# Performance work log

Hardware: AMD Instinct MI355X
Metric: run time of the kernel (lower is better)

## Reference

```python
import jax, jax.numpy as jnp
import numpy as np
import math

EMBED_DIM = 512
NUM_HEADS = 8
HEAD_DIM = EMBED_DIM // NUM_HEADS


def setup_inputs() -> dict:
    key = jax.random.key(0)
    ks = jax.random.split(key, 11)
    s = 1.0 / math.sqrt(EMBED_DIM)
    x = jax.random.normal(ks[0], (8, EMBED_DIM, 32, 32), dtype=jnp.float32)
    Wq = jax.random.uniform(ks[1], (EMBED_DIM, EMBED_DIM), jnp.float32, -s, s)
    bq = jax.random.uniform(ks[2], (EMBED_DIM,), jnp.float32, -s, s)
    Wk = jax.random.uniform(ks[3], (EMBED_DIM, EMBED_DIM), jnp.float32, -s, s)
    bk = jax.random.uniform(ks[4], (EMBED_DIM,), jnp.float32, -s, s)
    Wv = jax.random.uniform(ks[5], (EMBED_DIM, EMBED_DIM), jnp.float32, -s, s)
    bv = jax.random.uniform(ks[6], (EMBED_DIM,), jnp.float32, -s, s)
    Wo = jax.random.uniform(ks[7], (EMBED_DIM, EMBED_DIM), jnp.float32, -s, s)
    bo = jax.random.uniform(ks[8], (EMBED_DIM,), jnp.float32, -s, s)
    gamma = jnp.ones((EMBED_DIM,), jnp.float32)
    beta = jnp.zeros((EMBED_DIM,), jnp.float32)
    return {"x": x, "Wq": Wq, "bq": bq, "Wk": Wk, "bk": bk, "Wv": Wv,
            "bv": bv, "Wo": Wo, "bo": bo, "gamma": gamma, "beta": beta}


def layer_norm(x, gamma, beta, eps=1e-5):
    mu = jnp.mean(x, axis=-1, keepdims=True)
    var = jnp.mean(jnp.square(x - mu), axis=-1, keepdims=True)
    return (x - mu) * jax.lax.rsqrt(var + eps) * gamma + beta


def reference(x, Wq, bq, Wk, bk, Wv, bv, Wo, bo, gamma, beta):
    B, C, H, W = x.shape
    S = H * W
    # [B, S, C]
    x_flat = x.reshape(B, C, S).transpose(0, 2, 1)
    residual = x_flat
    xn = layer_norm(x_flat, gamma, beta)
    # torch Linear: y = x @ W^T + b
    q = (xn @ Wq.T + bq).reshape(B, S, NUM_HEADS, HEAD_DIM)
    k = (xn @ Wk.T + bk).reshape(B, S, NUM_HEADS, HEAD_DIM)
    v = (xn @ Wv.T + bv).reshape(B, S, NUM_HEADS, HEAD_DIM)
    scale = 1.0 / math.sqrt(HEAD_DIM)
    scores = jnp.einsum('bqhd,bkhd->bhqk', q, k) * scale
    attn = jax.nn.softmax(scores, axis=-1)  # dropout is identity in eval
    out = jnp.einsum('bhqk,bkhd->bqhd', attn, v).reshape(B, S, C)
    out = out @ Wo.T + bo + residual
    return out.transpose(0, 2, 1).reshape(B, C, H, W)
```

## Files before the change

kernel.cpp:

```cpp
#include <hip/hip_runtime.h>
#include <hip/hip_bf16.h>

typedef __bf16 bf16_t;
typedef __bf16 bf16x8 __attribute__((ext_vector_type(8)));
typedef float floatx4 __attribute__((ext_vector_type(4)));

#define EMBED 512
#define S_LEN 1024
#define NH 8
#define HD 64
#define LDK 1056
#define LDV 1088

#define MFMA16(a, b, c) __builtin_amdgcn_mfma_f32_16x16x32_bf16(a, b, c, 0, 0, 0)

static __device__ __forceinline__ bf16_t f2bf(float f) {
    unsigned int x = __builtin_bit_cast(unsigned int, f);
    unsigned int lsb = (x >> 16) & 1u;
    x += 0x7fffu + lsb;
    unsigned short u = (unsigned short)(x >> 16);
    return __builtin_bit_cast(bf16_t, u);
}
static __device__ __forceinline__ float bf2f(bf16_t v) {
    unsigned short u = __builtin_bit_cast(unsigned short, v);
    unsigned int x = ((unsigned int)u) << 16;
    return __builtin_bit_cast(float, x);
}
static __device__ __forceinline__ unsigned int pack2(float lo, float hi) {
    return (__builtin_bit_cast(unsigned int, lo) >> 16) |
           (__builtin_bit_cast(unsigned int, hi) & 0xFFFF0000u);
}
static __device__ __forceinline__ unsigned int pack2r(float lo, float hi) {
    unsigned short a = __builtin_bit_cast(unsigned short, f2bf(lo));
    unsigned short b = __builtin_bit_cast(unsigned short, f2bf(hi));
    return (unsigned int)a | ((unsigned int)b << 16);
}

__global__ __launch_bounds__(256) void cvt4_kernel(const float* __restrict__ s0,
                                                   const float* __restrict__ s1,
                                                   const float* __restrict__ s2,
                                                   const float* __restrict__ s3,
                                                   bf16_t* __restrict__ d0,
                                                   bf16_t* __restrict__ d1,
                                                   bf16_t* __restrict__ d2,
                                                   bf16_t* __restrict__ d3) {
    const float* s; bf16_t* d;
    switch (blockIdx.y) {
        case 0:  s = s0; d = d0; break;
        case 1:  s = s1; d = d1; break;
        case 2:  s = s2; d = d2; break;
        default: s = s3; d = d3; break;
    }
    int i = (blockIdx.x * 256 + threadIdx.x) * 8;
#pragma unroll
    for (int j = 0; j < 8; ++j) d[i + j] = f2bf(s[i + j]);
}

__global__ __launch_bounds__(256) void ln_fused_kernel(const float* __restrict__ x,
                                                       const float* __restrict__ gamma,
                                                       const float* __restrict__ beta,
                                                       bf16_t* __restrict__ xn) {
    __shared__ float T[32][521];
    __shared__ float Pm[32][33], Pq[32][33];
    __shared__ float Mu[32], Rs[32];
    int bid = blockIdx.x;
    int b = bid >> 5, s0 = (bid & 31) * 32;
    int t = threadIdx.x;
    int lc = t >> 3;
    int si = (t & 7) * 4;
    const float* xp = x + ((size_t)b * EMBED + lc) * S_LEN + s0 + si;
    float sm[4] = {}, sq[4] = {};
#pragma unroll
    for (int p = 0; p < 16; ++p) {
        int c = lc + p * 32;
        float4 v = *(const float4*)(xp + (size_t)p * 32 * S_LEN);
        int cs = c ^ ((c >> 3) & 0x38);
        T[si + 0][cs] = v.x; T[si + 1][cs] = v.y;
        T[si + 2][cs] = v.z; T[si + 3][cs] = v.w;
        sm[0] += v.x; sq[0] += v.x * v.x;
        sm[1] += v.y; sq[1] += v.y * v.y;
        sm[2] += v.z; sq[2] += v.z * v.z;
        sm[3] += v.w; sq[3] += v.w * v.w;
    }
#pragma unroll
    for (int k = 0; k < 4; ++k) { Pm[si + k][lc] = sm[k]; Pq[si + k][lc] = sq[k]; }
    __syncthreads();
    if (t < 32) {
        float m = 0.f, q = 0.f;
#pragma unroll
        for (int j = 0; j < 32; ++j) { m += Pm[t][j]; q += Pq[t][j]; }
        float mu = m * (1.0f / EMBED);
        float var = q * (1.0f / EMBED) - mu * mu;
        Mu[t] = mu; Rs[t] = rsqrtf(var + 1e-5f);
    }
    __syncthreads();
    int cidx = t & 31;
    int rw = t >> 5;
#pragma unroll
    for (int rg = 0; rg < 4; ++rg) {
        int srl = rg * 8 + rw;
        float mu = Mu[srl], rs = Rs[srl];
        int cb = cidx * 16;
        bf16_t* dst = xn + ((size_t)b * S_LEN + s0 + srl) * EMBED + cb;
#pragma unroll
        for (int h = 0; h < 2; ++h) {
            int c0h = cb + h * 8;
            float4 g0 = *(const float4*)(gamma + c0h);
            float4 g1 = *(const float4*)(gamma + c0h + 4);
            float4 be0 = *(const float4*)(beta + c0h);
            float4 be1 = *(const float4*)(beta + c0h + 4);
            float gv[8] = {g0.x, g0.y, g0.z, g0.w, g1.x, g1.y, g1.z, g1.w};
            float bv[8] = {be0.x, be0.y, be0.z, be0.w, be1.x, be1.y, be1.z, be1.w};
            bf16x8 o;
#pragma unroll
            for (int j = 0; j < 8; ++j) {
                int c = c0h + j;
                int cs = c ^ ((c >> 3) & 0x38);
                o[j] = f2bf((T[srl][cs] - mu) * rs * gv[j] + bv[j]);
            }
            *(bf16x8*)(dst + h * 8) = o;
        }
    }
}

__global__ __launch_bounds__(256) void gemm_kernel(const bf16_t* __restrict__ X,
                                                   const bf16_t* __restrict__ W,
                                                   const float* __restrict__ b0,
                                                   const float* __restrict__ b1,
                                                   const float* __restrict__ b2,
                                                   bf16_t* __restrict__ Y,
                                                   bf16_t* __restrict__ vtb) {
    __shared__ __align__(16) bf16_t Wl[2][128 * 72];
    int t = threadIdx.x;
    int col0 = blockIdx.y * 128, row0 = blockIdx.x * 128;
    int scol = t >> 1, sseg = (t & 1) * 32;
    const bf16_t* wsrc = W + (size_t)(col0 + scol) * EMBED + sseg;
    {
        bf16x8 r0 = *(const bf16x8*)(wsrc);
        bf16x8 r1 = *(const bf16x8*)(wsrc + 8);
        bf16x8 r2 = *(const bf16x8*)(wsrc + 16);
        bf16x8 r3 = *(const bf16x8*)(wsrc + 24);
        bf16_t* d = &Wl[0][scol * 72 + sseg];
        *(bf16x8*)d = r0;        *(bf16x8*)(d + 8) = r1;
        *(bf16x8*)(d + 16) = r2; *(bf16x8*)(d + 24) = r3;
    }
    int lane = t & 63, w = t >> 6, g = lane >> 4, n16 = lane & 15;
    int rw0 = row0 + w * 32;
    const bf16_t* xr0 = X + (size_t)(rw0 + n16) * EMBED + g * 8;
    const bf16_t* xr1 = xr0 + (size_t)16 * EMBED;
    bf16x8 a00 = *(const bf16x8*)(xr0);
    bf16x8 a01 = *(const bf16x8*)(xr0 + 32);
    bf16x8 a10 = *(const bf16x8*)(xr1);
    bf16x8 a11 = *(const bf16x8*)(xr1 + 32);
    __syncthreads();
    floatx4 acc[2][8] = {};
#pragma unroll
    for (int kc = 0; kc < 8; ++kc) {
        bf16x8 p0, p1, p2, p3, na00, na01, na10, na11;
        if (kc < 7) {
            int ko = (kc + 1) * 64;
            p0 = *(const bf16x8*)(wsrc + ko);
            p1 = *(const bf16x8*)(wsrc + ko + 8);
            p2 = *(const bf16x8*)(wsrc + ko + 16);
            p3 = *(const bf16x8*)(wsrc + ko + 24);
            na00 = *(const bf16x8*)(xr0 + ko);
            na01 = *(const bf16x8*)(xr0 + ko + 32);
            na10 = *(const bf16x8*)(xr1 + ko);
            na11 = *(const bf16x8*)(xr1 + ko + 32);
        }
        const bf16_t* wl = &Wl[kc & 1][0];
#pragma unroll
        for (int kk = 0; kk < 2; ++kk) {
            bf16x8 s0 = (kk == 0) ? a00 : a01;
            bf16x8 s1 = (kk == 0) ? a10 : a11;
#pragma unroll
            for (int nt = 0; nt < 8; ++nt) {
                bf16x8 bfr = *(const bf16x8*)(&wl[(nt * 16 + n16) * 72 + kk * 32 + g * 8]);
                acc[0][nt] = MFMA16(s0, bfr, acc[0][nt]);
                acc[1][nt] = MFMA16(s1, bfr, acc[1][nt]);
            }
        }
        if (kc < 7) {
            bf16_t* d = &Wl[(kc + 1) & 1][scol * 72 + sseg];
            *(bf16x8*)d = p0;        *(bf16x8*)(d + 8) = p1;
            *(bf16x8*)(d + 16) = p2; *(bf16x8*)(d + 24) = p3;
            a00 = na00; a01 = na01; a10 = na10; a11 = na11;
        }
        __syncthreads();
    }
    if (col0 < 1024) {
        const float* bp = (col0 < 512) ? b0 : b1;
#pragma unroll
        for (int ar = 0; ar < 2; ++ar)
#pragma unroll
            for (int nt = 0; nt < 8; ++nt) {
                int col = col0 + nt * 16 + n16;
                float bv = bp[col & 511];
#pragma unroll
                for (int r = 0; r < 4; ++r) {
                    int row = rw0 + ar * 16 + g * 4 + r;
                    Y[(size_t)row * LDK + col] = f2bf(acc[ar][nt][r] + bv);
                }
            }
    } else {
        bf16_t* Tl = &Wl[0][0];
#pragma unroll
        for (int ar = 0; ar < 2; ++ar)
#pragma unroll
            for (int nt = 0; nt < 8; ++nt) {
                int chl = nt * 16 + n16;
                float bv = b2[(col0 & 511) + chl];
                uint2 pr;
                pr.x = pack2r(acc[ar][nt][0] + bv, acc[ar][nt][1] + bv);
                pr.y = pack2r(acc[ar][nt][2] + bv, acc[ar][nt][3] + bv);
                *(uint2*)(&Tl[chl * 136 + w * 32 + ar * 16 + g * 4]) = pr;
            }
        __syncthreads();
        int ch = t >> 1, seg = (t & 1) * 64;
        int bb = row0 >> 10, s0 = row0 & 1023;
        bf16_t* dst = vtb + ((size_t)(bb * EMBED + (col0 - 1024) + ch)) * LDV + s0 + seg;
        const bf16_t* srcl = &Tl[ch * 136 + seg];
#pragma unroll
        for (int i = 0; i < 8; ++i)
            *(bf16x8*)(dst + i * 8) = *(const bf16x8*)(srcl + i * 8);
    }
}

__global__ __launch_bounds__(256) void wsgemm_out_kernel(const bf16_t* __restrict__ Wb,
                                                         const bf16_t* __restrict__ act,
                                                         const float* __restrict__ bias,
                                                         const float* __restrict__ xres,
                                                         float* __restrict__ out) {
    __shared__ __align__(16) bf16_t Al[2][64 * 72];
    int b = blockIdx.z, n0 = blockIdx.x * 64, m0 = blockIdx.y * 128;
    int t = threadIdx.x;
    int srow = t >> 2, sseg = (t & 3) * 16;
    const bf16_t* asrc = act + ((size_t)b * S_LEN + n0 + srow) * EMBED + sseg;
    {
        bf16x8 r0 = *(const bf16x8*)(asrc);
        bf16x8 r1 = *(const bf16x8*)(asrc + 8);
        bf16_t* d = &Al[0][srow * 72 + sseg];
        *(bf16x8*)d = r0; *(bf16x8*)(d + 8) = r1;
    }
    int lane = t & 63, w = t >> 6, g = lane >> 4, n16 = lane & 15;
    int mw = m0 + w * 32;
    const bf16_t* wr0 = Wb + (size_t)(mw + n16) * EMBED + g * 8;
    const bf16_t* wr1 = wr0 + (size_t)16 * EMBED;
    bf16x8 a00 = *(const bf16x8*)(wr0);
    bf16x8 a01 = *(const bf16x8*)(wr0 + 32);
    bf16x8 a10 = *(const bf16x8*)(wr1);
    bf16x8 a11 = *(const bf16x8*)(wr1 + 32);
    __syncthreads();
    floatx4 acc[2][4] = {};
#pragma unroll
    for (int kc = 0; kc < 8; ++kc) {
        bf16x8 p0, p1, na00, na01, na10, na11;
        if (kc < 7) {
            int ko = (kc + 1) * 64;
            p0 = *(const bf16x8*)(asrc + ko);
            p1 = *(const bf16x8*)(asrc + ko + 8);
            na00 = *(const bf16x8*)(wr0 + ko);
            na01 = *(const bf16x8*)(wr0 + ko + 32);
            na10 = *(const bf16x8*)(wr1 + ko);
            na11 = *(const bf16x8*)(wr1 + ko + 32);
        }
        const bf16_t* al = &Al[kc & 1][0];
#pragma unroll
        for (int kk = 0; kk < 2; ++kk) {
            bf16x8 s0 = (kk == 0) ? a00 : a01;
            bf16x8 s1 = (kk == 0) ? a10 : a11;
#pragma unroll
            for (int nt = 0; nt < 4; ++nt) {
                bf16x8 bfr = *(const bf16x8*)(&al[(nt * 16 + n16) * 72 + kk * 32 + g * 8]);
                acc[0][nt] = MFMA16(s0, bfr, acc[0][nt]);
                acc[1][nt] = MFMA16(s1, bfr, acc[1][nt]);
            }
        }
        if (kc < 7) {
            bf16_t* d = &Al[(kc + 1) & 1][srow * 72 + sseg];
            *(bf16x8*)d = p0; *(bf16x8*)(d + 8) = p1;
            a00 = na00; a01 = na01; a10 = na10; a11 = na11;
        }
        __syncthreads();
    }
#pragma unroll
    for (int ar = 0; ar < 2; ++ar)
#pragma unroll
        for (int r = 0; r < 4; ++r) {
            int row = mw + ar * 16 + g * 4 + r;
            float bv = bias[row];
#pragma unroll
            for (int nt = 0; nt < 4; ++nt) {
                int col = n0 + nt * 16 + n16;
                size_t oi = ((size_t)b * EMBED + row) * S_LEN + col;
                out[oi] = acc[ar][nt][r] + bv + xres[oi];
            }
        }
}

__global__ __launch_bounds__(256) void attn_kernel(const bf16_t* __restrict__ qk,
                                                   const bf16_t* __restrict__ vt,
                                                   bf16_t* __restrict__ o) {
    __shared__ __align__(16) bf16_t Kt[2][64 * 72];
    __shared__ __align__(16) unsigned int Pl[4][16 * 36];
    int bid = blockIdx.x;
    int bh = bid & 63, qt = bid >> 6;
    int b = bh >> 3, h = bh & 7;
    int t = threadIdx.x, w = t >> 6, lane = t & 63, g = lane >> 4, n16 = lane & 15;
    size_t baseQK = (size_t)b * S_LEN * LDK;
    size_t baseV  = ((size_t)b * EMBED + h * HD) * LDV;
    int qA = qt * 128 + w * 32 + n16;

    const float QSC = 0.18033688f;
    const bf16_t* qpA = qk + baseQK + (size_t)qA * LDK + h * HD + g * 8;
    const bf16_t* qpB = qpA + (size_t)16 * LDK;
    bf16x8 qa0 = *(const bf16x8*)(qpA);
    bf16x8 qa1 = *(const bf16x8*)(qpA + 32);
    bf16x8 qb0 = *(const bf16x8*)(qpB);
    bf16x8 qb1 = *(const bf16x8*)(qpB + 32);
#pragma unroll
    for (int j = 0; j < 8; ++j) {
        qa0[j] = f2bf(bf2f(qa0[j]) * QSC);
        qa1[j] = f2bf(bf2f(qa1[j]) * QSC);
        qb0[j] = f2bf(bf2f(qb0[j]) * QSC);
        qb1[j] = f2bf(bf2f(qb1[j]) * QSC);
    }
    const bf16_t* kbase = qk + baseQK + 512 + h * HD;
    const bf16_t* vbase = vt + baseV;

    int srow = t >> 2, scol = (t & 3) * 16;
    const bf16_t* ksrc = kbase + (size_t)srow * LDK + scol;
    {
        bf16x8 k0 = *(const bf16x8*)(ksrc);
        bf16x8 k1 = *(const bf16x8*)(ksrc + 8);
        bf16_t* kd = &Kt[0][srow * 72 + scol];
        *(bf16x8*)kd = k0; *(bf16x8*)(kd + 8) = k1;
    }

    float lsA[4] = {}, lsB[4] = {};
    floatx4 oaccA[4] = {}, oaccB[4] = {};
    unsigned int* PLw = &Pl[w][0];
    const float NEG12L2E = -17.3123405f;
    const float CLAMP    =  57.7078018f;

    for (int it = 0; it < 16; ++it) {
        int cur = it & 1, nxt = cur ^ 1;
        __syncthreads();
        bf16x8 vf0[4], vf1[4];
#pragma unroll
        for (int dt = 0; dt < 4; ++dt) {
            const bf16_t* vp = vbase + (size_t)(dt * 16 + n16) * LDV + it * 64 + g * 8;
            vf0[dt] = *(const bf16x8*)(vp);
            vf1[dt] = *(const bf16x8*)(vp + 32);
        }
        bf16x8 pk0, pk1;
        if (it < 15) {
            const bf16_t* kp = ksrc + (size_t)(it + 1) * 64 * LDK;
            pk0 = *(const bf16x8*)(kp);
            pk1 = *(const bf16x8*)(kp + 8);
        }
        const bf16_t* Kl = &Kt[cur][0];
        floatx4 sA[4], sB[4];
        __builtin_amdgcn_s_setprio(1);
#pragma unroll
        for (int kb = 0; kb < 4; ++kb) {
            bf16x8 k0 = *(const bf16x8*)(&Kl[(kb * 16 + n16) * 72 + g * 8]);
            bf16x8 k1 = *(const bf16x8*)(&Kl[(kb * 16 + n16) * 72 + 32 + g * 8]);
            sA[kb] = floatx4{NEG12L2E, NEG12L2E, NEG12L2E, NEG12L2E};
            sA[kb] = MFMA16(k0, qa0, sA[kb]);
            sA[kb] = MFMA16(k1, qa1, sA[kb]);
            sB[kb] = floatx4{NEG12L2E, NEG12L2E, NEG12L2E, NEG12L2E};
            sB[kb] = MFMA16(k0, qb0, sB[kb]);
            sB[kb] = MFMA16(k1, qb1, sB[kb]);
        }
        __builtin_amdgcn_s_setprio(0);
        if (it < 15) {
            bf16_t* kd = &Kt[nxt][srow * 72 + scol];
            *(bf16x8*)kd = pk0; *(bf16x8*)(kd + 8) = pk1;
        }
#pragma unroll
        for (int kb = 0; kb < 4; ++kb)
#pragma unroll
            for (int r = 0; r < 4; ++r) {
                float eA = exp2f(fminf(sA[kb][r], CLAMP));
                sA[kb][r] = eA; lsA[kb] += eA;
                float eB = exp2f(fminf(sB[kb][r], CLAMP));
                sB[kb][r] = eB; lsB[kb] += eB;
            }
#pragma unroll
        for (int kb = 0; kb < 4; ++kb) {
            uint2 pr;
            pr.x = pack2(sA[kb][0], sA[kb][1]);
            pr.y = pack2(sA[kb][2], sA[kb][3]);
            *(uint2*)&PLw[n16 * 36 + kb * 8 + g * 2] = pr;
        }
        uint4 uA0 = *(const uint4*)&PLw[n16 * 36 + g * 4];
        uint4 uA1 = *(const uint4*)&PLw[n16 * 36 + 16 + g * 4];
        bf16x8 pfA0 = __builtin_bit_cast(bf16x8, uA0);
        bf16x8 pfA1 = __builtin_bit_cast(bf16x8, uA1);
#pragma unroll
        for (int kb = 0; kb < 4; ++kb) {
            uint2 pr;
            pr.x = pack2(sB[kb][0], sB[kb][1]);
            pr.y = pack2(sB[kb][2], sB[kb][3]);
            *(uint2*)&PLw[n16 * 36 + kb * 8 + g * 2] = pr;
        }
        uint4 uB0 = *(const uint4*)&PLw[n16 * 36 + g * 4];
        uint4 uB1 = *(const uint4*)&PLw[n16 * 36 + 16 + g * 4];
        bf16x8 pfB0 = __builtin_bit_cast(bf16x8, uB0);
        bf16x8 pfB1 = __builtin_bit_cast(bf16x8, uB1);
        __builtin_amdgcn_s_setprio(1);
#pragma unroll
        for (int dt = 0; dt < 4; ++dt) {
            oaccA[dt] = MFMA16(vf0[dt], pfA0, oaccA[dt]);
            oaccA[dt] = MFMA16(vf1[dt], pfA1, oaccA[dt]);
            oaccB[dt] = MFMA16(vf0[dt], pfB0, oaccB[dt]);
            oaccB[dt] = MFMA16(vf1[dt], pfB1, oaccB[dt]);
        }
        __builtin_amdgcn_s_setprio(0);
    }
    float lA = (lsA[0] + lsA[1]) + (lsA[2] + lsA[3]);
    lA += __shfl_xor(lA, 16);
    lA += __shfl_xor(lA, 32);
    float lB = (lsB[0] + lsB[1]) + (lsB[2] + lsB[3]);
    lB += __shfl_xor(lB, 16);
    lB += __shfl_xor(lB, 32);
    float rlA = 1.0f / lA, rlB = 1.0f / lB;
    size_t orowA = ((size_t)b * S_LEN + qA) * EMBED + h * HD;
    size_t orowB = orowA + (size_t)16 * EMBED;
#pragma unroll
    for (int dt = 0; dt < 4; ++dt) {
        uint2 prA, prB;
        prA.x = pack2(oaccA[dt][0] * rlA, oaccA[dt][1] * rlA);
        prA.y = pack2(oaccA[dt][2] * rlA, oaccA[dt][3] * rlA);
        *(uint2*)(o + orowA + dt * 16 + g * 4) = prA;
        prB.x = pack2(oaccB[dt][0] * rlB, oaccB[dt][1] * rlB);
        prB.y = pack2(oaccB[dt][2] * rlB, oaccB[dt][3] * rlB);
        *(uint2*)(o + orowB + dt * 16 + g * 4) = prB;
    }
}

extern "C" void kernel_launch(void* const* d_in, const int* in_sizes, int n_in,
                              void* d_out, int out_size, void* d_ws, size_t ws_size,
                              hipStream_t stream) {
    const float* x     = (const float*)d_in[0];
    const float* Wq    = (const float*)d_in[1];
    const float* bq    = (const float*)d_in[2];
    const float* Wk    = (const float*)d_in[3];
    const float* bk    = (const float*)d_in[4];
    const float* Wv    = (const float*)d_in[5];
    const float* bv    = (const float*)d_in[6];
    const float* Wo    = (const float*)d_in[7];
    const float* bo    = (const float*)d_in[8];
    const float* gamma = (const float*)d_in[9];
    const float* beta  = (const float*)d_in[10];
    float* out = (float*)d_out;

    char* ws = (char*)d_ws;
    bf16_t* xn    = (bf16_t*)ws;
    bf16_t* qkb   = (bf16_t*)(ws + 8388608);
    bf16_t* wqkv  = (bf16_t*)(ws + 25690112);
    bf16_t* wo    = (bf16_t*)(ws + 27262976);
    bf16_t* ab    = xn;

    bf16_t* vtb = (bf16_t*)d_out;

    cvt4_kernel<<<dim3(128, 4), 256, 0, stream>>>(Wq, Wk, Wv, Wo,
                                                  wqkv, wqkv + 262144,
                                                  wqkv + 524288, wo);
    ln_fused_kernel<<<dim3(256), 256, 0, stream>>>(x, gamma, beta, xn);
    gemm_kernel<<<dim3(64, 12), 256, 0, stream>>>(xn, wqkv, bq, bk, bv, qkb, vtb);
    attn_kernel<<<dim3(512), 256, 0, stream>>>(qkb, vtb, ab);
    wsgemm_out_kernel<<<dim3(16, 4, 8), 256, 0, stream>>>(wo, ab, bo, x, out);
}
```

Before: 176.3 us.

## Split attention work across 8 waves with 16 queries each

The attention block grows from 4 to 8 waves, and each wave now handles a single 16-query tile instead of two. The K-tile staging is redistributed so each thread loads one 8-element vector. This halves per-wave register use and the length of the serial chain, and adds more waves to hide latency. In exchange, each V fragment loaded from global memory is reused by only one query tile per wave, which doubles V load traffic per query.

```diff
diff --git a/kernel.cpp b/kernel.cpp
--- a/kernel.cpp
+++ b/kernel.cpp
@@ -298,47 +298,41 @@
         }
 }
 
-__global__ __launch_bounds__(256) void attn_kernel(const bf16_t* __restrict__ qk,
-                                                   const bf16_t* __restrict__ vt,
-                                                   bf16_t* __restrict__ o) {
+__global__ __launch_bounds__(512, 4) void attn_kernel(const bf16_t* __restrict__ qk,
+                                                      const bf16_t* __restrict__ vt,
+                                                      bf16_t* __restrict__ o) {
     __shared__ __align__(16) bf16_t Kt[2][64 * 72];
-    __shared__ __align__(16) unsigned int Pl[4][16 * 36];
+    __shared__ __align__(16) unsigned int Pl[8][16 * 36];
     int bid = blockIdx.x;
     int bh = bid & 63, qt = bid >> 6;
     int b = bh >> 3, h = bh & 7;
     int t = threadIdx.x, w = t >> 6, lane = t & 63, g = lane >> 4, n16 = lane & 15;
     size_t baseQK = (size_t)b * S_LEN * LDK;
     size_t baseV  = ((size_t)b * EMBED + h * HD) * LDV;
-    int qA = qt * 128 + w * 32 + n16;
+    int qA = qt * 128 + w * 16 + n16;
 
     const float QSC = 0.18033688f;
     const bf16_t* qpA = qk + baseQK + (size_t)qA * LDK + h * HD + g * 8;
-    const bf16_t* qpB = qpA + (size_t)16 * LDK;
     bf16x8 qa0 = *(const bf16x8*)(qpA);
     bf16x8 qa1 = *(const bf16x8*)(qpA + 32);
-    bf16x8 qb0 = *(const bf16x8*)(qpB);
-    bf16x8 qb1 = *(const bf16x8*)(qpB + 32);
 #pragma unroll
     for (int j = 0; j < 8; ++j) {
         qa0[j] = f2bf(bf2f(qa0[j]) * QSC);
         qa1[j] = f2bf(bf2f(qa1[j]) * QSC);
-        qb0[j] = f2bf(bf2f(qb0[j]) * QSC);
-        qb1[j] = f2bf(bf2f(qb1[j]) * QSC);
     }
     const bf16_t* kbase = qk + baseQK + 512 + h * HD;
     const bf16_t* vbase = vt + baseV;
 
-    int srow = t >> 2, scol = (t & 3) * 16;
+    int srow = t >> 3, scol = (t & 7) * 8;
     const bf16_t* ksrc = kbase + (size_t)srow * LDK + scol;
     {
         bf16x8 k0 = *(const bf16x8*)(ksrc);
-        bf16x8 k1 = *(const bf16x8*)(ksrc + 8);
         bf16_t* kd = &Kt[0][srow * 72 + scol];
-        *(bf16x8*)kd = k0; *(bf16x8*)(kd + 8) = k1;
-    }
-
-    float lsA[4] = {}, lsB[4] = {};
-    floatx4 oaccA[4] = {}, oaccB[4] = {};
+        *(bf16x8*)kd = k0;
+    }
+
+    float lsA[4] = {};
+    floatx4 oaccA[4] = {};
     unsigned int* PLw = &Pl[w][0];
     const float NEG12L2E = -17.3123405f;
     const float CLAMP    =  57.7078018f;
@@ -353,14 +347,13 @@
             vf0[dt] = *(const bf16x8*)(vp);
             vf1[dt] = *(const bf16x8*)(vp + 32);
         }
-        bf16x8 pk0, pk1;
+        bf16x8 pk0;
         if (it < 15) {
             const bf16_t* kp = ksrc + (size_t)(it + 1) * 64 * LDK;
             pk0 = *(const bf16x8*)(kp);
-            pk1 = *(const bf16x8*)(kp + 8);
         }
         const bf16_t* Kl = &Kt[cur][0];
-        floatx4 sA[4], sB[4];
+        floatx4 sA[4];
         __builtin_amdgcn_s_setprio(1);
 #pragma unroll
         for (int kb = 0; kb < 4; ++kb) {
@@ -369,14 +362,11 @@
             sA[kb] = floatx4{NEG12L2E, NEG12L2E, NEG12L2E, NEG12L2E};
             sA[kb] = MFMA16(k0, qa0, sA[kb]);
             sA[kb] = MFMA16(k1, qa1, sA[kb]);
-            sB[kb] = floatx4{NEG12L2E, NEG12L2E, NEG12L2E, NEG12L2E};
-            sB[kb] = MFMA16(k0, qb0, sB[kb]);
-            sB[kb] = MFMA16(k1, qb1, sB[kb]);
         }
         __builtin_amdgcn_s_setprio(0);
         if (it < 15) {
             bf16_t* kd = &Kt[nxt][srow * 72 + scol];
-            *(bf16x8*)kd = pk0; *(bf16x8*)(kd + 8) = pk1;
+            *(bf16x8*)kd = pk0;
         }
 #pragma unroll
         for (int kb = 0; kb < 4; ++kb)
@@ -384,8 +374,6 @@
             for (int r = 0; r < 4; ++r) {
                 float eA = exp2f(fminf(sA[kb][r], CLAMP));
                 sA[kb][r] = eA; lsA[kb] += eA;
-                float eB = exp2f(fminf(sB[kb][r], CLAMP));
-                sB[kb][r] = eB; lsB[kb] += eB;
             }
 #pragma unroll
         for (int kb = 0; kb < 4; ++kb) {
@@ -398,45 +386,25 @@
         uint4 uA1 = *(const uint4*)&PLw[n16 * 36 + 16 + g * 4];
         bf16x8 pfA0 = __builtin_bit_cast(bf16x8, uA0);
         bf16x8 pfA1 = __builtin_bit_cast(bf16x8, uA1);
-#pragma unroll
-        for (int kb = 0; kb < 4; ++kb) {
-            uint2 pr;
-            pr.x = pack2(sB[kb][0], sB[kb][1]);
-            pr.y = pack2(sB[kb][2], sB[kb][3]);
-            *(uint2*)&PLw[n16 * 36 + kb * 8 + g * 2] = pr;
-        }
-        uint4 uB0 = *(const uint4*)&PLw[n16 * 36 + g * 4];
-        uint4 uB1 = *(const uint4*)&PLw[n16 * 36 + 16 + g * 4];
-        bf16x8 pfB0 = __builtin_bit_cast(bf16x8, uB0);
-        bf16x8 pfB1 = __builtin_bit_cast(bf16x8, uB1);
         __builtin_amdgcn_s_setprio(1);
 #pragma unroll
         for (int dt = 0; dt < 4; ++dt) {
             oaccA[dt] = MFMA16(vf0[dt], pfA0, oaccA[dt]);
             oaccA[dt] = MFMA16(vf1[dt], pfA1, oaccA[dt]);
-            oaccB[dt] = MFMA16(vf0[dt], pfB0, oaccB[dt]);
-            oaccB[dt] = MFMA16(vf1[dt], pfB1, oaccB[dt]);
         }
         __builtin_amdgcn_s_setprio(0);
     }
     float lA = (lsA[0] + lsA[1]) + (lsA[2] + lsA[3]);
     lA += __shfl_xor(lA, 16);
     lA += __shfl_xor(lA, 32);
-    float lB = (lsB[0] + lsB[1]) + (lsB[2] + lsB[3]);
-    lB += __shfl_xor(lB, 16);
-    lB += __shfl_xor(lB, 32);
-    float rlA = 1.0f / lA, rlB = 1.0f / lB;
+    float rlA = 1.0f / lA;
     size_t orowA = ((size_t)b * S_LEN + qA) * EMBED + h * HD;
-    size_t orowB = orowA + (size_t)16 * EMBED;
 #pragma unroll
     for (int dt = 0; dt < 4; ++dt) {
-        uint2 prA, prB;
+        uint2 prA;
         prA.x = pack2(oaccA[dt][0] * rlA, oaccA[dt][1] * rlA);
         prA.y = pack2(oaccA[dt][2] * rlA, oaccA[dt][3] * rlA);
         *(uint2*)(o + orowA + dt * 16 + g * 4) = prA;
-        prB.x = pack2(oaccB[dt][0] * rlB, oaccB[dt][1] * rlB);
-        prB.y = pack2(oaccB[dt][2] * rlB, oaccB[dt][3] * rlB);
-        *(uint2*)(o + orowB + dt * 16 + g * 4) = prB;
     }
 }
 
@@ -470,6 +438,6 @@
                                                   wqkv + 524288, wo);
     ln_fused_kernel<<<dim3(256), 256, 0, stream>>>(x, gamma, beta, xn);
     gemm_kernel<<<dim3(64, 12), 256, 0, stream>>>(xn, wqkv, bq, bk, bv, qkb, vtb);
-    attn_kernel<<<dim3(512), 256, 0, stream>>>(qkb, vtb, ab);
+    attn_kernel<<<dim3(512), 512, 0, stream>>>(qkb, vtb, ab);
     wsgemm_out_kernel<<<dim3(16, 4, 8), 256, 0, stream>>>(wo, ab, bo, x, out);
 }
```

Measured after the change: 198.4 us. 12.5% more time.
